# Performance work log

Measured on AMD Instinct MI355X. Metric: run time of the kernel, lower is better.

## Reference

```python
import jax, jax.numpy as jnp
import numpy as np

B, S, D, H = 2, 2048, 2048, 16
Dh = D // H


def _rotate_interleaved(t):
    # t: (..., Dh); pairs (x0,x1) -> (-x1, x0), interleaved
    t2 = t.reshape(t.shape[:-1] + (Dh // 2, 2))
    rot = jnp.stack([-t2[..., 1], t2[..., 0]], axis=-1)
    return rot.reshape(t.shape)


def _apply_rope(t, cos, sin):
    # t: (B,H,S,Dh); cos/sin: (S,Dh) broadcast over batch and heads
    return t * cos[None, None, :, :] + _rotate_interleaved(t) * sin[None, None, :, :]


def setup_inputs() -> dict:
    key = jax.random.key(0)
    ks = jax.random.split(key, 4)
    x = jax.random.normal(ks[0], (B, S, D), dtype=jnp.float32)
    wq = jax.random.normal(ks[1], (D, D), dtype=jnp.float32) * (D ** -0.5)
    wk = jax.random.normal(ks[2], (D, D), dtype=jnp.float32) * (D ** -0.5)
    wv = jax.random.normal(ks[3], (D, D), dtype=jnp.float32) * (D ** -0.5)
    # Real RoPE cos/sin tables: theta_i = 10000^{-2i/Dh}, interleaved layout
    inv_freq = 1.0 / (10000.0 ** (np.arange(0, Dh, 2, dtype=np.float32) / Dh))
    angles = np.arange(S, dtype=np.float32)[:, None] * inv_freq[None, :]  # (S, Dh/2)
    angles = np.repeat(angles, 2, axis=-1)  # (S, Dh) interleaved
    rope_cos = jnp.asarray(np.cos(angles))
    rope_sin = jnp.asarray(np.sin(angles))
    return {"x": x, "wq": wq, "wk": wk, "wv": wv,
            "rope_cos": rope_cos, "rope_sin": rope_sin}


def reference(x, wq, wk, wv, rope_cos, rope_sin):
    b, s, d = x.shape
    # QKV projections (torch Linear: y = x @ W^T), split into heads -> (B,H,S,Dh)
    def proj(w):
        return (x @ w.T).reshape(b, s, H, Dh).transpose(0, 2, 1, 3)
    q, k, v = proj(wq), proj(wk), proj(wv)
    cos, sin = rope_cos[:s], rope_sin[:s]
    q = _apply_rope(q, cos, sin)
    k = _apply_rope(k, cos, sin)
    # causal SDPA
    scores = jnp.einsum('bhqd,bhkd->bhqk', q, k) / jnp.sqrt(jnp.float32(Dh))
    causal = jnp.tril(jnp.ones((s, s), dtype=bool))
    scores = jnp.where(causal[None, None], scores, jnp.float32(-1e30))
    attn = jax.nn.softmax(scores, axis=-1)
    out = jnp.einsum('bhqk,bhkd->bhqd', attn, v)  # (B,H,S,Dh)
    # extra trailing softmax over head dim (as in source)
    out = jax.nn.softmax(out.astype(jnp.float32), axis=-1)
    return out.transpose(0, 2, 1, 3).reshape(b, s, -1)
```

## Files before the change

kernel.cpp:

```cpp
#include <hip/hip_runtime.h>

#define Bc 2
#define Sc 2048
#define Dc 2048
#define Hc 16
#define DHc 128

typedef _Float16 f16;
typedef __attribute__((ext_vector_type(4))) _Float16 v4h;
typedef __attribute__((ext_vector_type(8))) _Float16 v8h;
typedef __attribute__((ext_vector_type(4))) float v4f;
typedef __attribute__((ext_vector_type(16))) float v16f;
typedef __attribute__((ext_vector_type(4))) float f32x4;

__global__ void cvt_kernel(const float* __restrict__ x, const float* __restrict__ wq,
                           const float* __restrict__ wk, const float* __restrict__ wv,
                           f16* __restrict__ xh, f16* __restrict__ wqh,
                           f16* __restrict__ wkh, f16* __restrict__ wvh)
{
    int bid = blockIdx.x;
    const float* src; f16* dst; int idx;
    if (bid < 8192)       { src = x;  dst = xh;  idx = bid; }
    else if (bid < 12288) { src = wq; dst = wqh; idx = bid - 8192; }
    else if (bid < 16384) { src = wk; dst = wkh; idx = bid - 12288; }
    else                  { src = wv; dst = wvh; idx = bid - 16384; }
    int i = idx * 256 + threadIdx.x;
    f32x4 v = ((const f32x4*)src)[i];
    v4h hv; hv[0]=(f16)v[0]; hv[1]=(f16)v[1]; hv[2]=(f16)v[2]; hv[3]=(f16)v[3];
    ((v4h*)dst)[i] = hv;
}

__launch_bounds__(512, 2)
__global__ void proj256_kernel(const f16* __restrict__ xh, const f16* __restrict__ wall,
                               const float* __restrict__ cs, const float* __restrict__ sn,
                               f16* __restrict__ qh, f16* __restrict__ kh,
                               f16* __restrict__ vt)
{
    const int bid = blockIdx.x;
    const int swz = (bid & 7) * 96 + (bid >> 3);
    const int mt = swz & 31, nt = swz >> 5;
    const int m0 = mt * 128, n0 = nt * 256;

    const int tid = threadIdx.x;
    const int wid = tid >> 6, lane = tid & 63;
    const int wr = wid >> 2, wc = wid & 3;
    const int l15 = lane & 15, quad = lane >> 4;
    const int x7 = l15 & 7;

    __shared__ __align__(16) f16 lds[49152];

    const f16* aS[2]; const f16* bS[4];
    #pragma unroll
    for (int j = 0; j < 2; ++j) {
        int c = tid + j * 512;
        int r = c >> 3, s = c & 7;
        aS[j] = xh + (size_t)(m0 + r) * Dc + ((s ^ (r & 7)) * 8);
    }
    #pragma unroll
    for (int j = 0; j < 4; ++j) {
        int c = tid + j * 512;
        int r = c >> 3, s = c & 7;
        bS[j] = wall + (size_t)(n0 + r) * Dc + ((s ^ (r & 7)) * 8);
    }

#define STAGE(kt_, buf_) do {                                                   \
        const int _ko = (kt_) * 64;                                             \
        f16* _b = lds + (buf_) * 24576;                                         \
        _Pragma("unroll")                                                       \
        for (int j = 0; j < 2; ++j)                                             \
            __builtin_amdgcn_global_load_lds(                                   \
                (const __attribute__((address_space(1))) void*)(aS[j] + _ko),   \
                (__attribute__((address_space(3))) void*)(_b + j * 4096 + wid * 512), \
                16, 0, 0);                                                      \
        _Pragma("unroll")                                                       \
        for (int j = 0; j < 4; ++j)                                             \
            __builtin_amdgcn_global_load_lds(                                   \
                (const __attribute__((address_space(1))) void*)(bS[j] + _ko),   \
                (__attribute__((address_space(3))) void*)(_b + 8192 + j * 4096 + wid * 512), \
                16, 0, 0);                                                      \
    } while (0)

#define RDFRAG(af_, bf_, buf_) do {                                             \
        const f16* _Ab = lds + (buf_) * 24576;                                  \
        const f16* _Bb = _Ab + 8192;                                            \
        _Pragma("unroll")                                                       \
        for (int kk = 0; kk < 2; ++kk) {                                        \
            _Pragma("unroll")                                                   \
            for (int mi = 0; mi < 4; ++mi)                                      \
                af_[kk][mi] = *(const v8h*)(_Ab + (wr * 64 + mi * 16 + l15) * 64 \
                                            + (((kk * 4 + quad) ^ x7) * 8));    \
            _Pragma("unroll")                                                   \
            for (int ni = 0; ni < 4; ++ni)                                      \
                bf_[kk][ni] = *(const v8h*)(_Bb + (wc * 64 + ni * 16 + l15) * 64 \
                                            + (((kk * 4 + quad) ^ x7) * 8));    \
        }                                                                       \
    } while (0)

#define MM(af_, bf_) do {                                                       \
        __builtin_amdgcn_s_setprio(1);                                          \
        _Pragma("unroll")                                                       \
        for (int kk = 0; kk < 2; ++kk)                                          \
            _Pragma("unroll")                                                   \
            for (int mi = 0; mi < 4; ++mi)                                      \
                _Pragma("unroll")                                               \
                for (int ni = 0; ni < 4; ++ni)                                  \
                    acc[mi][ni] = __builtin_amdgcn_mfma_f32_16x16x32_f16(       \
                        af_[kk][mi], bf_[kk][ni], acc[mi][ni], 0, 0, 0);        \
        __builtin_amdgcn_s_setprio(0);                                          \
    } while (0)

    v4f acc[4][4];
    #pragma unroll
    for (int i = 0; i < 4; ++i)
        #pragma unroll
        for (int j = 0; j < 4; ++j)
            acc[i][j] = (v4f){0.f, 0.f, 0.f, 0.f};

    v8h afA[2][4], bfA[2][4], afB[2][4], bfB[2][4];

    STAGE(0, 0);
    STAGE(1, 1);
    __syncthreads();
    RDFRAG(afA, bfA, 0);
    __syncthreads();

    #pragma unroll 1
    for (int t = 0; t < 32; t += 2) {
        if (t + 2 < 32) STAGE(t + 2, 0);
        RDFRAG(afB, bfB, 1);
        MM(afA, bfA);
        __syncthreads();
        if (t + 3 < 32) STAGE(t + 3, 1);
        if (t + 2 < 32) RDFRAG(afA, bfA, 0);
        MM(afB, bfB);
        __syncthreads();
    }

#undef STAGE
#undef RDFRAG
#undef MM

    const int z = n0 >> 11;
    const int bb = m0 >> 11, s0 = m0 & 2047;

    if (z < 2) {
        f16 (*Ep)[264] = (f16(*)[264])lds;
        #pragma unroll
        for (int mi = 0; mi < 4; ++mi)
            #pragma unroll
            for (int ni = 0; ni < 4; ++ni)
                #pragma unroll
                for (int r = 0; r < 4; ++r)
                    Ep[wr * 64 + mi * 16 + quad * 4 + r][wc * 64 + ni * 16 + l15] =
                        (f16)acc[mi][ni][r];
        __syncthreads();
        f16* outp = (z == 0) ? qh : kh;
        const float scl = (z == 0) ? 0.08838834764831845f : 1.0f;
        #pragma unroll
        for (int it = 0; it < 8; ++it) {
            int ch = tid + it * 512, row = ch >> 5, c = ch & 31;
            v8h val = *(const v8h*)&Ep[row][c * 8];
            int s = s0 + row;
            int nn = (n0 & 2047) + c * 8;
            int h = nn >> 7, d0 = nn & 127;
            const float* cp = cs + (size_t)s * DHc + d0;
            const float* sp = sn + (size_t)s * DHc + d0;
            f32x4 ca = *(const f32x4*)cp, cb = *(const f32x4*)(cp + 4);
            f32x4 sa = *(const f32x4*)sp, sb = *(const f32x4*)(sp + 4);
            float v[8];
            #pragma unroll
            for (int j = 0; j < 8; ++j) v[j] = (float)val[j];
            v8h rv;
            rv[0] = (f16)((v[0]*ca[0] - v[1]*sa[0]) * scl);
            rv[1] = (f16)((v[1]*ca[1] + v[0]*sa[1]) * scl);
            rv[2] = (f16)((v[2]*ca[2] - v[3]*sa[2]) * scl);
            rv[3] = (f16)((v[3]*ca[3] + v[2]*sa[3]) * scl);
            rv[4] = (f16)((v[4]*cb[0] - v[5]*sb[0]) * scl);
            rv[5] = (f16)((v[5]*cb[1] + v[4]*sb[1]) * scl);
            rv[6] = (f16)((v[6]*cb[2] - v[7]*sb[2]) * scl);
            rv[7] = (f16)((v[7]*cb[3] + v[6]*sb[3]) * scl);
            *(v8h*)(outp + ((size_t)(bb * Hc + h) * Sc + s) * DHc + d0) = rv;
        }
    } else {
        f16 (*Ep)[136] = (f16(*)[136])lds;
        #pragma unroll
        for (int mi = 0; mi < 4; ++mi)
            #pragma unroll
            for (int ni = 0; ni < 4; ++ni)
                #pragma unroll
                for (int r = 0; r < 4; ++r)
                    Ep[wc * 64 + ni * 16 + l15][wr * 64 + mi * 16 + quad * 4 + r] =
                        (f16)acc[mi][ni][r];
        __syncthreads();
        #pragma unroll
        for (int it = 0; it < 8; ++it) {
            int ch = tid + it * 512, n = ch >> 4, cm = ch & 15;
            int nn = (n0 & 2047) + n;
            int h = nn >> 7, d = nn & 127;
            int s = s0 + cm * 8;
            *(v8h*)(vt + ((size_t)(bb * Hc + h) * DHc + d) * Sc + s) =
                *(const v8h*)&Ep[n][cm * 8];
        }
    }
}

__launch_bounds__(256)
__global__ void proj_kernel(const float* __restrict__ x, const float* __restrict__ wq,
                            const float* __restrict__ wk, const float* __restrict__ wv,
                            f16* __restrict__ qh, f16* __restrict__ kh, f16* __restrict__ vt)
{
    const int z = blockIdx.z;
    const float* w = (z == 0) ? wq : ((z == 1) ? wk : wv);
    const int m0 = blockIdx.x * 128, n0 = blockIdx.y * 128;
    const int tid = threadIdx.x, lane = tid & 63, wid = tid >> 6;
    const int wm = wid >> 1, wn = wid & 1;
    const int l15 = lane & 15, quad = lane >> 4;

    __shared__ __align__(16) f16 smem[2 * 128 * 72];
    f16 (*As)[72] = (f16(*)[72])smem;
    f16 (*Bs)[72] = (f16(*)[72])(smem + 128 * 72);

    v4f acc[4][4];
    for (int i = 0; i < 4; ++i)
        for (int j = 0; j < 4; ++j)
            acc[i][j] = (v4f){0.f, 0.f, 0.f, 0.f};

    for (int k0 = 0; k0 < Dc; k0 += 64) {
        __syncthreads();
        for (int it = 0; it < 4; ++it) {
            int chunk = tid + it * 256;
            int r = chunk >> 3, cc = chunk & 7;
            const f32x4* pa = (const f32x4*)(x + (size_t)(m0 + r) * Dc + k0 + cc * 8);
            f32x4 a0 = pa[0], a1 = pa[1];
            v8h ha;
            ha[0]=(f16)a0[0]; ha[1]=(f16)a0[1]; ha[2]=(f16)a0[2]; ha[3]=(f16)a0[3];
            ha[4]=(f16)a1[0]; ha[5]=(f16)a1[1]; ha[6]=(f16)a1[2]; ha[7]=(f16)a1[3];
            *(v8h*)&As[r][cc * 8] = ha;
            const f32x4* pb = (const f32x4*)(w + (size_t)(n0 + r) * Dc + k0 + cc * 8);
            f32x4 b0 = pb[0], b1 = pb[1];
            v8h hb;
            hb[0]=(f16)b0[0]; hb[1]=(f16)b0[1]; hb[2]=(f16)b0[2]; hb[3]=(f16)b0[3];
            hb[4]=(f16)b1[0]; hb[5]=(f16)b1[1]; hb[6]=(f16)b1[2]; hb[7]=(f16)b1[3];
            *(v8h*)&Bs[r][cc * 8] = hb;
        }
        __syncthreads();
        for (int kk = 0; kk < 2; ++kk) {
            v8h af[4], bf[4];
            for (int mi = 0; mi < 4; ++mi)
                af[mi] = *(const v8h*)&As[wm * 64 + mi * 16 + l15][kk * 32 + quad * 8];
            for (int ni = 0; ni < 4; ++ni)
                bf[ni] = *(const v8h*)&Bs[wn * 64 + ni * 16 + l15][kk * 32 + quad * 8];
            for (int mi = 0; mi < 4; ++mi)
                for (int ni = 0; ni < 4; ++ni)
                    acc[mi][ni] = __builtin_amdgcn_mfma_f32_16x16x32_f16(
                        af[mi], bf[ni], acc[mi][ni], 0, 0, 0);
        }
    }
    __syncthreads();
    f16 (*Ep)[136] = (f16(*)[136])smem;
    for (int mi = 0; mi < 4; ++mi)
        for (int ni = 0; ni < 4; ++ni)
            for (int r = 0; r < 4; ++r) {
                int ml = wm * 64 + mi * 16 + quad * 4 + r;
                int nl = wn * 64 + ni * 16 + l15;
                f16 val = (f16)acc[mi][ni][r];
                if (z == 2) Ep[nl][ml] = val;
                else        Ep[ml][nl] = val;
            }
    __syncthreads();
    const int b = m0 >> 11, s0 = m0 & 2047, h = n0 >> 7;
    if (z < 2) {
        f16* outp = (z == 0) ? qh : kh;
        for (int it = 0; it < 8; ++it) {
            int ch = tid + it * 256, row = ch >> 4, c = ch & 15;
            *(v8h*)(outp + ((size_t)((b * Hc + h) * Sc) + s0 + row) * DHc + c * 8) =
                *(const v8h*)&Ep[row][c * 8];
        }
    } else {
        for (int it = 0; it < 8; ++it) {
            int ch = tid + it * 256, row = ch >> 4, c = ch & 15;
            *(v8h*)(vt + ((size_t)((b * Hc + h) * DHc) + row) * Sc + s0 + c * 8) =
                *(const v8h*)&Ep[row][c * 8];
        }
    }
}

__global__ void rope_kernel(f16* __restrict__ qh, f16* __restrict__ kh,
                            const float* __restrict__ cs, const float* __restrict__ sn)
{
    int i  = blockIdx.x * 256 + threadIdx.x;
    int d2 = i & 63;
    int s  = (i >> 6) & (Sc - 1);
    int bh = i >> 17;
    f16* t = blockIdx.y ? kh : qh;
    float scale = blockIdx.y ? 1.0f : 0.08838834764831845f;
    float c  = cs[s * DHc + 2 * d2];
    float sv = sn[s * DHc + 2 * d2];
    f16* p = t + ((size_t)bh * Sc + s) * DHc + 2 * d2;
    float t0 = (float)p[0], t1 = (float)p[1];
    p[0] = (f16)((t0 * c - t1 * sv) * scale);
    p[1] = (f16)((t1 * c + t0 * sv) * scale);
}

__launch_bounds__(256, 2)
__global__ void attn_kernel(const f16* __restrict__ qh, const f16* __restrict__ kh,
                            const f16* __restrict__ vt, float* __restrict__ out)
{
    const int L = blockIdx.x;
    const int slot = L >> 3;
    const int bh = (L & 7) * 4 + (slot >> 3);
    const int p  = slot & 7;
    const int b = bh >> 4, h = bh & 15;
    const int tid = threadIdx.x, lane = tid & 63, w = tid >> 6;
    const int l31 = lane & 31, half = lane >> 5;
    const int sw = l31 & 7;

    __shared__ __align__(16) f16 smem[32768];
    f16* ksm = smem;
    f16* vsm = smem + 16384;

    const size_t bhoff = (size_t)bh * Sc * DHc;

    const f16* ksrc[4]; const f16* vsrc[4];
    f16* kdst[4]; f16* vdst[4];
    #pragma unroll
    for (int j = 0; j < 4; ++j) {
        int slot0 = j * 256 + w * 64;
        {   int r = (slot0 >> 4) + (lane >> 4);
            int c = (lane & 15) ^ (r & 7);
            ksrc[j] = kh + bhoff + (size_t)r * DHc + c * 8;
            kdst[j] = ksm + slot0 * 8; }
        {   int r = (slot0 >> 3) + (lane >> 3);
            int c = (lane & 7) ^ (r & 7);
            vsrc[j] = vt + bhoff + (size_t)r * Sc + c * 8;
            vdst[j] = vsm + slot0 * 8; }
    }

#define STAGE(kt_, buf_) do {                                                   \
        int _ko = (kt_) * 64 * DHc;                                             \
        int _vo = (kt_) * 64;                                                   \
        int _lb = (buf_) * 8192;                                                \
        _Pragma("unroll")                                                       \
        for (int j = 0; j < 4; ++j) {                                           \
            __builtin_amdgcn_global_load_lds(                                   \
                (const __attribute__((address_space(1))) void*)(ksrc[j] + _ko), \
                (__attribute__((address_space(3))) void*)(kdst[j] + _lb), 16, 0, 0); \
            __builtin_amdgcn_global_load_lds(                                   \
                (const __attribute__((address_space(1))) void*)(vsrc[j] + _vo), \
                (__attribute__((address_space(3))) void*)(vdst[j] + _lb), 16, 0, 0); \
        } } while (0)

    const int qtA = 15 - p;
    const int nktA = 2 * qtA + 2;

    int ibuf = 0;
    STAGE(0, 0);

    #pragma unroll 1
    for (int ph = 0; ph < 2; ++ph) {
        const int qt  = ph ? p : qtA;
        const int nkt = 2 * qt + 2;
        const int q0  = qt * 128 + w * 32;
        const int qg  = q0 + l31;

        v8h qf[8];
        const f16* qrow = qh + bhoff + (size_t)qg * DHc;
        #pragma unroll
        for (int s = 0; s < 8; ++s)
            qf[s] = *(const v8h*)(qrow + s * 16 + half * 8);

        float l_run = 0.f;
        v16f o[4];
        #pragma unroll
        for (int i = 0; i < 4; ++i)
            #pragma unroll
            for (int r = 0; r < 16; ++r) o[i][r] = 0.f;

        #pragma unroll 1
        for (int kt = 0; kt < nkt; ++kt, ++ibuf) {
            __syncthreads();
            const int buf = ibuf & 1;
            const int ni = ibuf + 1;
            if (ni < 34) {
                int tn = (ni < nktA) ? ni : ni - nktA;
                STAGE(tn, ni & 1);
            }
            if (q0 + 31 < kt * 64) continue;

            const f16* kbuf = ksm + buf * 8192;
            const f16* vbuf = vsm + buf * 8192;
            const bool do1 = (kt * 64 + 32 <= q0 + 31);

            v16f st0, st1;
            #pragma unroll
            for (int r = 0; r < 16; ++r) { st0[r] = 0.f; st1[r] = 0.f; }
            #pragma unroll
            for (int s = 0; s < 8; ++s) {
                int c = ((s * 2 + half) ^ sw) * 8;
                v8h kf0 = *(const v8h*)(kbuf + l31 * 128 + c);
                st0 = __builtin_amdgcn_mfma_f32_32x32x16_f16(kf0, qf[s], st0, 0, 0, 0);
                if (do1) {
                    v8h kf1 = *(const v8h*)(kbuf + (32 + l31) * 128 + c);
                    st1 = __builtin_amdgcn_mfma_f32_32x32x16_f16(kf1, qf[s], st1, 0, 0, 0);
                }
            }

            float sum = 0.f;
            #pragma unroll
            for (int r = 0; r < 16; ++r) {
                int key = kt * 64 + (r & 3) + 8 * (r >> 2) + 4 * half;
                float sv = (key > qg) ? -1e30f : st0[r];
                float pe = __expf(sv);
                st0[r] = pe; sum += pe;
            }
            if (do1) {
                #pragma unroll
                for (int r = 0; r < 16; ++r) {
                    int key = kt * 64 + 32 + (r & 3) + 8 * (r >> 2) + 4 * half;
                    float sv = (key > qg) ? -1e30f : st1[r];
                    float pe = __expf(sv);
                    st1[r] = pe; sum += pe;
                }
            }
            sum += __shfl_xor(sum, 32);
            l_run += sum;

            #pragma unroll
            for (int s2 = 0; s2 < 4; ++s2) {
                v4h bfr;
                bfr[0]=(f16)st0[4*s2]; bfr[1]=(f16)st0[4*s2+1];
                bfr[2]=(f16)st0[4*s2+2]; bfr[3]=(f16)st0[4*s2+3];
                int c = ((s2 ^ sw) * 8) + half * 4;
                #pragma unroll
                for (int dt = 0; dt < 4; ++dt) {
                    v4h vf = *(const v4h*)(vbuf + (dt * 32 + l31) * 64 + c);
                    o[dt] = __builtin_amdgcn_mfma_f32_32x32x8f16(vf, bfr, o[dt], 0, 0, 0);
                }
            }
            if (do1) {
                #pragma unroll
                for (int s2 = 0; s2 < 4; ++s2) {
                    v4h bfr;
                    bfr[0]=(f16)st1[4*s2]; bfr[1]=(f16)st1[4*s2+1];
                    bfr[2]=(f16)st1[4*s2+2]; bfr[3]=(f16)st1[4*s2+3];
                    int c = (((4 + s2) ^ sw) * 8) + half * 4;
                    #pragma unroll
                    for (int dt = 0; dt < 4; ++dt) {
                        v4h vf = *(const v4h*)(vbuf + (dt * 32 + l31) * 64 + c);
                        o[dt] = __builtin_amdgcn_mfma_f32_32x32x8f16(vf, bfr, o[dt], 0, 0, 0);
                    }
                }
            }
        }

        float inv = 1.f / l_run;
        float mxd = -1e30f;
        #pragma unroll
        for (int dt = 0; dt < 4; ++dt)
            #pragma unroll
            for (int r = 0; r < 16; ++r) {
                o[dt][r] *= inv;
                mxd = fmaxf(mxd, o[dt][r]);
            }
        mxd = fmaxf(mxd, __shfl_xor(mxd, 32));
        float sd = 0.f;
        #pragma unroll
        for (int dt = 0; dt < 4; ++dt)
            #pragma unroll
            for (int r = 0; r < 16; ++r) {
                float t = __expf(o[dt][r] - mxd);
                o[dt][r] = t;
                sd += t;
            }
        sd += __shfl_xor(sd, 32);
        float rinv = 1.f / sd;

        float* orow = out + (size_t)(b * Sc + qg) * Dc + h * DHc;
        #pragma unroll
        for (int dt = 0; dt < 4; ++dt)
            #pragma unroll
            for (int g = 0; g < 4; ++g) {
                f32x4 vv;
                vv[0] = o[dt][4*g+0] * rinv;
                vv[1] = o[dt][4*g+1] * rinv;
                vv[2] = o[dt][4*g+2] * rinv;
                vv[3] = o[dt][4*g+3] * rinv;
                *(f32x4*)(orow + dt * 32 + g * 8 + half * 4) = vv;
            }
    }
#undef STAGE
}

extern "C" void kernel_launch(void* const* d_in, const int* in_sizes, int n_in,
                              void* d_out, int out_size, void* d_ws, size_t ws_size,
                              hipStream_t stream)
{
    const float* x  = (const float*)d_in[0];
    const float* wq = (const float*)d_in[1];
    const float* wk = (const float*)d_in[2];
    const float* wv = (const float*)d_in[3];
    const float* cs = (const float*)d_in[4];
    const float* sn = (const float*)d_in[5];
    float* out = (float*)d_out;

    const size_t tsz = (size_t)Bc * Hc * Sc * DHc;
    f16* qh = (f16*)d_ws;
    f16* kh = qh + tsz;
    f16* vt = kh + tsz;

    if (ws_size >= 11 * tsz) {
        f16* xh  = vt + tsz;
        f16* wqh = xh + tsz;
        f16* wkh = wqh + tsz / 2;
        f16* wvh = wkh + tsz / 2;
        cvt_kernel<<<20480, 256, 0, stream>>>(x, wq, wk, wv, xh, wqh, wkh, wvh);
        proj256_kernel<<<768, 512, 0, stream>>>(xh, wqh, cs, sn, qh, kh, vt);
    } else {
        proj_kernel<<<dim3(32, 16, 3), 256, 0, stream>>>(x, wq, wk, wv, qh, kh, vt);
        rope_kernel<<<dim3(16384, 2), 256, 0, stream>>>(qh, kh, cs, sn);
    }
    attn_kernel<<<256, 256, 0, stream>>>(qh, kh, vt, out);
}
```

Measured before the change: 342.0 us.

## Triple-buffer projection GEMM LDS stages with explicit vmcnt waits

Grows the projection GEMM's shared-memory staging from two to three buffers so global loads run two k-tiles ahead. Full __syncthreads are replaced by explicit s_waitcnt vmcnt/lgkmcnt counts plus raw barriers, so the kernel waits only for the tile it is about to read. This aims to hide global-load latency behind MFMA work. LDS use per block rises from 96KB to 144KB, which may cut occupancy below the launch bound of two blocks, and the hand-counted waits are fragile if the number of loads per stage changes.

Result: slower. 493.8 us (+44.4%).

```diff
diff --git a/kernel.cpp b/kernel.cpp
--- a/kernel.cpp
+++ b/kernel.cpp
@@ -47,7 +47,7 @@
     const int l15 = lane & 15, quad = lane >> 4;
     const int x7 = l15 & 7;
 
-    __shared__ __align__(16) f16 lds[49152];
+    __shared__ __align__(16) f16 lds[73728];
 
     const f16* aS[2]; const f16* bS[4];
     #pragma unroll
@@ -109,6 +109,12 @@
         __builtin_amdgcn_s_setprio(0);                                          \
     } while (0)
 
+#define VMW12 asm volatile("s_waitcnt vmcnt(12)" ::: "memory")
+#define VMW6  asm volatile("s_waitcnt vmcnt(6)"  ::: "memory")
+#define VMW0  asm volatile("s_waitcnt vmcnt(0)"  ::: "memory")
+#define LGKM0 asm volatile("s_waitcnt lgkmcnt(0)" ::: "memory")
+#define BAR   __builtin_amdgcn_s_barrier()
+
     v4f acc[4][4];
     #pragma unroll
     for (int i = 0; i < 4; ++i)
@@ -120,25 +126,50 @@
 
     STAGE(0, 0);
     STAGE(1, 1);
-    __syncthreads();
+    STAGE(2, 2);
+    VMW12;
+    BAR;
     RDFRAG(afA, bfA, 0);
-    __syncthreads();
+    LGKM0;
+    BAR;
 
     #pragma unroll 1
     for (int t = 0; t < 32; t += 2) {
-        if (t + 2 < 32) STAGE(t + 2, 0);
-        RDFRAG(afB, bfB, 1);
+        const int bufc  = t % 3;
+        const int bufn  = (t + 1) % 3;
+        const int bufn2 = (t + 2) % 3;
+
+        if (t + 3 < 32) STAGE(t + 3, bufc);
+        if (t <= 28) { VMW12; } else { VMW0; }
+        BAR;
+        RDFRAG(afB, bfB, bufn);
         MM(afA, bfA);
-        __syncthreads();
-        if (t + 3 < 32) STAGE(t + 3, 1);
-        if (t + 2 < 32) RDFRAG(afA, bfA, 0);
-        MM(afB, bfB);
-        __syncthreads();
+        LGKM0;
+        BAR;
+
+        if (t + 4 < 32) STAGE(t + 4, bufn);
+        if (t + 2 < 32) {
+            if (t <= 26) { VMW12; } else { VMW6; }
+            BAR;
+            RDFRAG(afA, bfA, bufn2);
+            MM(afB, bfB);
+            LGKM0;
+            BAR;
+        } else {
+            MM(afB, bfB);
+        }
     }
 
 #undef STAGE
 #undef RDFRAG
 #undef MM
+#undef VMW12
+#undef VMW6
+#undef VMW0
+#undef LGKM0
+#undef BAR
+
+    __syncthreads();
 
     const int z = n0 >> 11;
     const int bb = m0 >> 11, s0 = m0 & 2047;
```

## Triple-buffer projection GEMM LDS with explicit vmcnt waits and split-K fragment reads

Applied to the files above, without the earlier changes.

Moves the QKV projection GEMM from two LDS stages to three rotating buffers. Global-to-LDS loads are issued two tiles ahead, and partial s_waitcnt vmcnt waits plus raw s_barrier replace the full __syncthreads. Fragment reads are split per k-half so LDS reads of the second half overlap the MFMAs of the first. This aims to hide global load latency and cut barrier stalls, but LDS use grows to 144KB per block, which may reduce occupancy under launch_bounds(512,2).

Measured after the change: 316.2 us. -7.6%, faster.

```diff
diff --git a/kernel.cpp b/kernel.cpp
--- a/kernel.cpp
+++ b/kernel.cpp
@@ -47,7 +47,7 @@
     const int l15 = lane & 15, quad = lane >> 4;
     const int x7 = l15 & 7;
 
-    __shared__ __align__(16) f16 lds[49152];
+    __shared__ __align__(16) f16 lds[73728];
 
     const f16* aS[2]; const f16* bS[4];
     #pragma unroll
@@ -63,51 +63,49 @@
         bS[j] = wall + (size_t)(n0 + r) * Dc + ((s ^ (r & 7)) * 8);
     }
 
+#define GLD(src_, dst_)                                                         \
+    __builtin_amdgcn_global_load_lds(                                           \
+        (const __attribute__((address_space(1))) void*)(src_),                  \
+        (__attribute__((address_space(3))) void*)(dst_), 16, 0, 0)
+
 #define STAGE(kt_, buf_) do {                                                   \
         const int _ko = (kt_) * 64;                                             \
         f16* _b = lds + (buf_) * 24576;                                         \
-        _Pragma("unroll")                                                       \
-        for (int j = 0; j < 2; ++j)                                             \
-            __builtin_amdgcn_global_load_lds(                                   \
-                (const __attribute__((address_space(1))) void*)(aS[j] + _ko),   \
-                (__attribute__((address_space(3))) void*)(_b + j * 4096 + wid * 512), \
-                16, 0, 0);                                                      \
-        _Pragma("unroll")                                                       \
-        for (int j = 0; j < 4; ++j)                                             \
-            __builtin_amdgcn_global_load_lds(                                   \
-                (const __attribute__((address_space(1))) void*)(bS[j] + _ko),   \
-                (__attribute__((address_space(3))) void*)(_b + 8192 + j * 4096 + wid * 512), \
-                16, 0, 0);                                                      \
+        GLD(aS[0] + _ko, _b + wid * 512);                                       \
+        GLD(aS[1] + _ko, _b + 4096 + wid * 512);                                \
+        GLD(bS[0] + _ko, _b + 8192 + wid * 512);                                \
+        GLD(bS[1] + _ko, _b + 8192 + 4096  + wid * 512);                        \
+        GLD(bS[2] + _ko, _b + 8192 + 8192  + wid * 512);                        \
+        GLD(bS[3] + _ko, _b + 8192 + 12288 + wid * 512);                        \
     } while (0)
 
-#define RDFRAG(af_, bf_, buf_) do {                                             \
+#define RDF(af_, bf_, buf_, kk_) do {                                           \
         const f16* _Ab = lds + (buf_) * 24576;                                  \
         const f16* _Bb = _Ab + 8192;                                            \
         _Pragma("unroll")                                                       \
-        for (int kk = 0; kk < 2; ++kk) {                                        \
-            _Pragma("unroll")                                                   \
-            for (int mi = 0; mi < 4; ++mi)                                      \
-                af_[kk][mi] = *(const v8h*)(_Ab + (wr * 64 + mi * 16 + l15) * 64 \
-                                            + (((kk * 4 + quad) ^ x7) * 8));    \
-            _Pragma("unroll")                                                   \
-            for (int ni = 0; ni < 4; ++ni)                                      \
-                bf_[kk][ni] = *(const v8h*)(_Bb + (wc * 64 + ni * 16 + l15) * 64 \
-                                            + (((kk * 4 + quad) ^ x7) * 8));    \
-        }                                                                       \
+        for (int mi = 0; mi < 4; ++mi)                                          \
+            af_[mi] = *(const v8h*)(_Ab + (wr * 64 + mi * 16 + l15) * 64        \
+                                    + ((((kk_) * 4 + quad) ^ x7) * 8));         \
+        _Pragma("unroll")                                                       \
+        for (int ni = 0; ni < 4; ++ni)                                          \
+            bf_[ni] = *(const v8h*)(_Bb + (wc * 64 + ni * 16 + l15) * 64        \
+                                    + ((((kk_) * 4 + quad) ^ x7) * 8));         \
     } while (0)
 
 #define MM(af_, bf_) do {                                                       \
         __builtin_amdgcn_s_setprio(1);                                          \
         _Pragma("unroll")                                                       \
-        for (int kk = 0; kk < 2; ++kk)                                          \
+        for (int mi = 0; mi < 4; ++mi)                                          \
             _Pragma("unroll")                                                   \
-            for (int mi = 0; mi < 4; ++mi)                                      \
-                _Pragma("unroll")                                               \
-                for (int ni = 0; ni < 4; ++ni)                                  \
-                    acc[mi][ni] = __builtin_amdgcn_mfma_f32_16x16x32_f16(       \
-                        af_[kk][mi], bf_[kk][ni], acc[mi][ni], 0, 0, 0);        \
+            for (int ni = 0; ni < 4; ++ni)                                      \
+                acc[mi][ni] = __builtin_amdgcn_mfma_f32_16x16x32_f16(           \
+                    af_[mi], bf_[ni], acc[mi][ni], 0, 0, 0);                    \
         __builtin_amdgcn_s_setprio(0);                                          \
     } while (0)
+
+#define VMW6  asm volatile("s_waitcnt vmcnt(6)"  ::: "memory")
+#define VMW0  asm volatile("s_waitcnt vmcnt(0)"  ::: "memory")
+#define BARM  asm volatile("s_barrier" ::: "memory")
 
     v4f acc[4][4];
     #pragma unroll
@@ -116,29 +114,39 @@
         for (int j = 0; j < 4; ++j)
             acc[i][j] = (v4f){0.f, 0.f, 0.f, 0.f};
 
-    v8h afA[2][4], bfA[2][4], afB[2][4], bfB[2][4];
+    v8h af0[4], bf0[4], af1[4], bf1[4];
 
     STAGE(0, 0);
     STAGE(1, 1);
+    VMW6;
+    BARM;
+    RDF(af0, bf0, 0, 0);
+
+    int bR = 0, bN = 1, bS2 = 2;
+
+    #pragma unroll 1
+    for (int t = 0; t < 32; ++t) {
+        BARM;
+        if (t + 2 < 32) STAGE(t + 2, bS2);
+        RDF(af1, bf1, bR, 1);
+        MM(af0, bf0);
+        if (t + 1 < 32) {
+            if (t + 2 < 32) { VMW6; } else { VMW0; }
+            BARM;
+            RDF(af0, bf0, bN, 0);
+        }
+        MM(af1, bf1);
+        int tmp = bR; bR = bN; bN = bS2; bS2 = tmp;
+    }
     __syncthreads();
-    RDFRAG(afA, bfA, 0);
-    __syncthreads();
-
-    #pragma unroll 1
-    for (int t = 0; t < 32; t += 2) {
-        if (t + 2 < 32) STAGE(t + 2, 0);
-        RDFRAG(afB, bfB, 1);
-        MM(afA, bfA);
-        __syncthreads();
-        if (t + 3 < 32) STAGE(t + 3, 1);
-        if (t + 2 < 32) RDFRAG(afA, bfA, 0);
-        MM(afB, bfB);
-        __syncthreads();
-    }
 
 #undef STAGE
-#undef RDFRAG
+#undef GLD
+#undef RDF
 #undef MM
+#undef VMW6
+#undef VMW0
+#undef BARM
 
     const int z = n0 >> 11;
     const int bb = m0 >> 11, s0 = m0 & 2047;
```

## Load A fragments directly to registers and triple-buffer B tiles in LDS

Applied to the files above, without the earlier changes.

The QKV projection GEMM no longer stages the x tile through LDS. Each wave loads its A fragments straight from global memory into registers, one k-step ahead. The B (weight) tiles move from a two-buffer to a three-slot LDS ring, with a manual vmcnt wait and s_barrier replacing __syncthreads. This aims to cut LDS traffic and barrier stalls, at the cost of redundant global reads of A across the column waves and a fragile hand-tuned waitcnt count.

After: 440.0 us. 28.6% more time.

```diff
diff --git a/kernel.cpp b/kernel.cpp
--- a/kernel.cpp
+++ b/kernel.cpp
@@ -49,13 +49,7 @@
 
     __shared__ __align__(16) f16 lds[49152];
 
-    const f16* aS[2]; const f16* bS[4];
-    #pragma unroll
-    for (int j = 0; j < 2; ++j) {
-        int c = tid + j * 512;
-        int r = c >> 3, s = c & 7;
-        aS[j] = xh + (size_t)(m0 + r) * Dc + ((s ^ (r & 7)) * 8);
-    }
+    const f16* bS[4];
     #pragma unroll
     for (int j = 0; j < 4; ++j) {
         int c = tid + j * 512;
@@ -63,40 +57,45 @@
         bS[j] = wall + (size_t)(n0 + r) * Dc + ((s ^ (r & 7)) * 8);
     }
 
-#define STAGE(kt_, buf_) do {                                                   \
+    const f16* aP[4];
+    #pragma unroll
+    for (int mi = 0; mi < 4; ++mi)
+        aP[mi] = xh + (size_t)(m0 + wr * 64 + mi * 16 + l15) * Dc + quad * 8;
+
+#define GLD(src_, dst_)                                                         \
+    __builtin_amdgcn_global_load_lds(                                           \
+        (const __attribute__((address_space(1))) void*)(src_),                  \
+        (__attribute__((address_space(3))) void*)(dst_), 16, 0, 0)
+
+#define STAGE_B(kt_, slot_) do {                                                \
         const int _ko = (kt_) * 64;                                             \
-        f16* _b = lds + (buf_) * 24576;                                         \
+        f16* _b = lds + (slot_) * 16384;                                        \
+        GLD(bS[0] + _ko, _b + wid * 512);                                       \
+        GLD(bS[1] + _ko, _b + 4096  + wid * 512);                               \
+        GLD(bS[2] + _ko, _b + 8192  + wid * 512);                               \
+        GLD(bS[3] + _ko, _b + 12288 + wid * 512);                               \
+    } while (0)
+
+#define LOAD_A(set_, kt_) do {                                                  \
+        const int _ko = (kt_) * 64;                                             \
         _Pragma("unroll")                                                       \
-        for (int j = 0; j < 2; ++j)                                             \
-            __builtin_amdgcn_global_load_lds(                                   \
-                (const __attribute__((address_space(1))) void*)(aS[j] + _ko),   \
-                (__attribute__((address_space(3))) void*)(_b + j * 4096 + wid * 512), \
-                16, 0, 0);                                                      \
+        for (int mi = 0; mi < 4; ++mi) {                                        \
+            set_[0][mi] = *(const v8h*)(aP[mi] + _ko);                          \
+            set_[1][mi] = *(const v8h*)(aP[mi] + _ko + 32);                     \
+        }                                                                       \
+    } while (0)
+
+#define RDB(bf_, slot_) do {                                                    \
+        const f16* _Bb = lds + (slot_) * 16384;                                 \
         _Pragma("unroll")                                                       \
-        for (int j = 0; j < 4; ++j)                                             \
-            __builtin_amdgcn_global_load_lds(                                   \
-                (const __attribute__((address_space(1))) void*)(bS[j] + _ko),   \
-                (__attribute__((address_space(3))) void*)(_b + 8192 + j * 4096 + wid * 512), \
-                16, 0, 0);                                                      \
-    } while (0)
-
-#define RDFRAG(af_, bf_, buf_) do {                                             \
-        const f16* _Ab = lds + (buf_) * 24576;                                  \
-        const f16* _Bb = _Ab + 8192;                                            \
-        _Pragma("unroll")                                                       \
-        for (int kk = 0; kk < 2; ++kk) {                                        \
-            _Pragma("unroll")                                                   \
-            for (int mi = 0; mi < 4; ++mi)                                      \
-                af_[kk][mi] = *(const v8h*)(_Ab + (wr * 64 + mi * 16 + l15) * 64 \
-                                            + (((kk * 4 + quad) ^ x7) * 8));    \
+        for (int kk = 0; kk < 2; ++kk)                                          \
             _Pragma("unroll")                                                   \
             for (int ni = 0; ni < 4; ++ni)                                      \
                 bf_[kk][ni] = *(const v8h*)(_Bb + (wc * 64 + ni * 16 + l15) * 64 \
                                             + (((kk * 4 + quad) ^ x7) * 8));    \
-        }                                                                       \
     } while (0)
 
-#define MM(af_, bf_) do {                                                       \
+#define MM(a_, bf_) do {                                                        \
         __builtin_amdgcn_s_setprio(1);                                          \
         _Pragma("unroll")                                                       \
         for (int kk = 0; kk < 2; ++kk)                                          \
@@ -105,9 +104,12 @@
                 _Pragma("unroll")                                               \
                 for (int ni = 0; ni < 4; ++ni)                                  \
                     acc[mi][ni] = __builtin_amdgcn_mfma_f32_16x16x32_f16(       \
-                        af_[kk][mi], bf_[kk][ni], acc[mi][ni], 0, 0, 0);        \
+                        a_[kk][mi], bf_[kk][ni], acc[mi][ni], 0, 0, 0);         \
         __builtin_amdgcn_s_setprio(0);                                          \
     } while (0)
+
+#define VMW12 asm volatile("s_waitcnt vmcnt(12)" ::: "memory")
+#define BARM  asm volatile("s_barrier" ::: "memory")
 
     v4f acc[4][4];
     #pragma unroll
@@ -116,29 +118,51 @@
         for (int j = 0; j < 4; ++j)
             acc[i][j] = (v4f){0.f, 0.f, 0.f, 0.f};
 
-    v8h afA[2][4], bfA[2][4], afB[2][4], bfB[2][4];
-
-    STAGE(0, 0);
-    STAGE(1, 1);
+    v8h a0[2][4], a1[2][4];
+
+    STAGE_B(0, 0);
+    STAGE_B(1, 1);
+    LOAD_A(a0, 0);
+    VMW12;
+    BARM;
+
+    int bR = 0, bSt = 2;
+
+    #pragma unroll 1
+    for (int tt = 0; tt < 32; tt += 2) {
+        if (tt + 2 < 32) STAGE_B(tt + 2, bSt);
+        LOAD_A(a1, tt + 1);
+        {
+            v8h bf[2][4];
+            RDB(bf, bR);
+            MM(a0, bf);
+        }
+        VMW12;
+        BARM;
+        bR = (bR == 2) ? 0 : bR + 1;
+        bSt = (bSt == 2) ? 0 : bSt + 1;
+
+        if (tt + 3 < 32) STAGE_B(tt + 3, bSt);
+        if (tt + 2 < 32) LOAD_A(a0, tt + 2);
+        {
+            v8h bf[2][4];
+            RDB(bf, bR);
+            MM(a1, bf);
+        }
+        VMW12;
+        BARM;
+        bR = (bR == 2) ? 0 : bR + 1;
+        bSt = (bSt == 2) ? 0 : bSt + 1;
+    }
     __syncthreads();
-    RDFRAG(afA, bfA, 0);
-    __syncthreads();
-
-    #pragma unroll 1
-    for (int t = 0; t < 32; t += 2) {
-        if (t + 2 < 32) STAGE(t + 2, 0);
-        RDFRAG(afB, bfB, 1);
-        MM(afA, bfA);
-        __syncthreads();
-        if (t + 3 < 32) STAGE(t + 3, 1);
-        if (t + 2 < 32) RDFRAG(afA, bfA, 0);
-        MM(afB, bfB);
-        __syncthreads();
-    }
-
-#undef STAGE
-#undef RDFRAG
+
+#undef STAGE_B
+#undef LOAD_A
+#undef GLD
+#undef RDB
 #undef MM
+#undef VMW12
+#undef BARM
 
     const int z = n0 >> 11;
     const int bb = m0 >> 11, s0 = m0 & 2047;
```
